# Kernel tuning notes

Hardware: AMD Instinct MI355X
Metric: run time of the kernel (lower is better)

Reference implementation:

```python
import jax, jax.numpy as jnp
import numpy as np

N0, N1, N2, C = 100_000, 400_000, 300_000, 128
NNZ1, NNZ2 = 2 * N1, 3 * N2  # 2 boundary nodes per edge, 3 boundary edges per triangle


def setup_inputs() -> dict:
    key = jax.random.key(0)
    ks = jax.random.split(key, 11)
    x0 = jax.random.normal(ks[0], (N0, C), dtype=jnp.float32)
    x1 = jax.random.normal(ks[1], (N1, C), dtype=jnp.float32)
    x2 = jax.random.normal(ks[2], (N2, C), dtype=jnp.float32)  # unused by the math (rank-2 conv reads rank-1 feats)
    W1 = jax.random.normal(ks[3], (C, C), dtype=jnp.float32) / np.sqrt(C)
    W2 = jax.random.normal(ks[4], (C, C), dtype=jnp.float32) / np.sqrt(C)
    # COO of incidence B_1: (N0, N1); B_2: (N1, N2)
    b1_rows = jax.random.randint(ks[5], (NNZ1,), 0, N0, dtype=jnp.int32)
    b1_cols = jax.random.randint(ks[6], (NNZ1,), 0, N1, dtype=jnp.int32)
    b1_vals = jax.random.uniform(ks[7], (NNZ1,), dtype=jnp.float32)
    b2_rows = jax.random.randint(ks[8], (NNZ2,), 0, N1, dtype=jnp.int32)
    b2_cols = jax.random.randint(ks[9], (NNZ2,), 0, N2, dtype=jnp.int32)
    b2_vals = jax.random.uniform(ks[10], (NNZ2,), dtype=jnp.float32)
    return {"x0": x0, "x1": x1, "x2": x2, "W1": W1, "W2": W2,
            "b1_rows": b1_rows, "b1_cols": b1_cols, "b1_vals": b1_vals,
            "b2_rows": b2_rows, "b2_cols": b2_cols, "b2_vals": b2_vals}


def _conv_low_to_high(x, W, rows, cols, vals, n_out):
    # B_r^T @ (x @ W): rows index (r-1)-cells (source), cols index r-cells (dest).
    h = x @ W                              # (n_{r-1}, C) dense GEMM
    msg = h[rows] * vals[:, None]          # (nnz, C) gather + scale
    return jax.ops.segment_sum(msg, cols, num_segments=n_out)  # (n_r, C)


def reference(x0, x1, x2, W1, W2, b1_rows, b1_cols, b1_vals, b2_rows, b2_cols, b2_vals):
    # Aggregation of a single-message list with aggr_func="sum" is identity,
    # followed by the sigmoid update. Rank 0 has an empty message list (the
    # original torch code would crash there), so outputs are ranks 1..max_rank.
    out1 = jax.nn.sigmoid(_conv_low_to_high(x0, W1, b1_rows, b1_cols, b1_vals, N1))
    out2 = jax.nn.sigmoid(_conv_low_to_high(x1, W2, b2_rows, b2_cols, b2_vals, N2))
    return (out1, out2)
```

## Files before the change

### kernel.cpp

```cpp
#include <hip/hip_runtime.h>
#include <hip/hip_bf16.h>

#define CDIM 128
#define SCAN_CHUNK 2048

typedef __attribute__((ext_vector_type(4))) float f32x4;
typedef __attribute__((ext_vector_type(8))) short bf16x8;
typedef __attribute__((ext_vector_type(4))) short bf16x4;

__device__ __forceinline__ short f2bf(float f) {
    unsigned u = __float_as_uint(f);
    u += 0x7FFFu + ((u >> 16) & 1u);
    return (short)(u >> 16);
}


__global__ __launch_bounds__(256) void zero_ints(int* __restrict__ p, int n) {
    int i = blockIdx.x * 256 + threadIdx.x;
    for (; i < n; i += gridDim.x * 256) p[i] = 0;
}

__global__ __launch_bounds__(256) void hist_both(
    const int* __restrict__ c1, int nnz1, const int* __restrict__ c2, int nnz2,
    int n1, int* __restrict__ counts)
{
    const int gtid = blockIdx.x * 256 + threadIdx.x;
    const int gstride = gridDim.x * 256;
    for (int e = gtid; e < nnz1; e += gstride) atomicAdd(&counts[c1[e]], 1);
    for (int e = gtid; e < nnz2; e += gstride) atomicAdd(&counts[n1 + c2[e]], 1);
}

__global__ __launch_bounds__(256) void scan_chunks(const int* __restrict__ in, int* __restrict__ out,
                                                   int* __restrict__ bsums, int n) {
    __shared__ int wtot[4];
    const int t = threadIdx.x;
    const int base = blockIdx.x * SCAN_CHUNK + t * 8;
    int v[8]; int s = 0;
#pragma unroll
    for (int j = 0; j < 8; ++j) {
        int c = (base + j < n) ? in[base + j] : 0;
        v[j] = s; s += c;
    }
    const int lane = t & 63, w = t >> 6;
    int inc = s;
#pragma unroll
    for (int d = 1; d < 64; d <<= 1) {
        int o = __shfl_up(inc, d);
        if (lane >= d) inc += o;
    }
    if (lane == 63) wtot[w] = inc;
    __syncthreads();
    int off = inc - s;
    for (int i = 0; i < w; ++i) off += wtot[i];
#pragma unroll
    for (int j = 0; j < 8; ++j)
        if (base + j < n) out[base + j] = v[j] + off;
    if (t == 255) bsums[blockIdx.x] = off + s;
}

__global__ __launch_bounds__(256) void scan_finalize(int* __restrict__ row_ptr,
                                                     const int* __restrict__ bsums,
                                                     int* __restrict__ cursor, int n, int nnzT) {
    __shared__ int wsum[4];
    const int t = threadIdx.x, lane = t & 63, w = t >> 6;
    int s = 0;
    for (int i = t; i < (int)blockIdx.x; i += 256) s += bsums[i];
#pragma unroll
    for (int d = 1; d < 64; d <<= 1) s += __shfl_xor(s, d);
    if (lane == 0) wsum[w] = s;
    __syncthreads();
    const int off = wsum[0] + wsum[1] + wsum[2] + wsum[3];
    const int base = blockIdx.x * SCAN_CHUNK + t * 8;
#pragma unroll
    for (int j = 0; j < 8; ++j) {
        const int i = base + j;
        if (i < n) {
            int val = row_ptr[i] + off;
            row_ptr[i] = val;
            cursor[i] = val;
        }
    }
    if (blockIdx.x == 0 && t == 0) row_ptr[n] = nnzT;
}

__global__ __launch_bounds__(256) void scatter_gemm(
    const int* __restrict__ r1, const int* __restrict__ c1, const float* __restrict__ v1, int nnz1,
    const int* __restrict__ r2, const int* __restrict__ c2, const float* __restrict__ v2, int nnz2,
    int n1, int* __restrict__ cursor, unsigned long long* __restrict__ csr, int nscat,
    const float* __restrict__ x0, const float* __restrict__ W1, short* __restrict__ h0, int t0,
    const float* __restrict__ x1, const float* __restrict__ W2, short* __restrict__ h1, int t1,
    int g0)
{
    __shared__ short Bfrag[4][8][64][8];

    if ((int)blockIdx.x < nscat) {
        const int gtid = blockIdx.x * 256 + threadIdx.x;
        const int gstride = nscat * 256;
        for (int e = gtid; e < nnz1; e += gstride) {
            int p = atomicAdd(&cursor[c1[e]], 1);
            csr[p] = ((unsigned long long)__float_as_uint(__builtin_nontemporal_load(&v1[e])) << 32)
                     | (unsigned)__builtin_nontemporal_load(&r1[e]);
        }
        for (int e = gtid; e < nnz2; e += gstride) {
            int p = atomicAdd(&cursor[n1 + c2[e]], 1);
            csr[p] = ((unsigned long long)__float_as_uint(__builtin_nontemporal_load(&v2[e])) << 32)
                     | (unsigned)__builtin_nontemporal_load(&r2[e]);
        }
        return;
    }

    const int gb = blockIdx.x - nscat;
    const float* __restrict__ x; const float* __restrict__ W; short* __restrict__ h;
    int ntiles, bidx, nblk;
    const int ngemm = gridDim.x - nscat;
    if (gb < g0) { x = x0; W = W1; h = h0; ntiles = t0; bidx = gb;      nblk = g0; }
    else         { x = x1; W = W2; h = h1; ntiles = t1; bidx = gb - g0; nblk = ngemm - g0; }

    for (int slot = threadIdx.x; slot < 2048; slot += 256) {
        const int lane = slot & 63, nb = (slot >> 6) & 7, kk = slot >> 9;
        const int n  = nb * 16 + (lane & 15);
        const int k0 = kk * 32 + (lane >> 4) * 8;
        union { bf16x8 v; short s[8]; } f;
#pragma unroll
        for (int j = 0; j < 8; ++j) f.s[j] = f2bf(W[(k0 + j) * CDIM + n]);
        *(bf16x8*)&Bfrag[kk][nb][lane][0] = f.v;
    }
    __syncthreads();

    const int lane = threadIdx.x & 63;
    const int wid  = threadIdx.x >> 6;
    const int l15  = lane & 15;
    const int l4   = lane >> 4;

    for (int tile = bidx * 4 + wid; tile < ntiles; tile += nblk * 4) {
        const int rbase = tile << 4;
        const int row = rbase + l15;
        const float* __restrict__ xr = x + (long)row * CDIM + (l4 << 3);

        union { bf16x8 v; short s[8]; } X[4];
#pragma unroll
        for (int kk = 0; kk < 4; ++kk) {
            f32x4 a0 = __builtin_nontemporal_load((const f32x4*)(xr + kk * 32));
            f32x4 a1 = __builtin_nontemporal_load((const f32x4*)(xr + kk * 32 + 4));
#pragma unroll
            for (int j = 0; j < 4; ++j) { X[kk].s[j] = f2bf(a0[j]); X[kk].s[4 + j] = f2bf(a1[j]); }
        }

        f32x4 c[8];
#pragma unroll
        for (int nb = 0; nb < 8; ++nb) c[nb] = (f32x4){0.f, 0.f, 0.f, 0.f};
#pragma unroll
        for (int kk = 0; kk < 4; ++kk)
#pragma unroll
            for (int nb = 0; nb < 8; ++nb)
                c[nb] = __builtin_amdgcn_mfma_f32_16x16x32_bf16(
                            *(const bf16x8*)&Bfrag[kk][nb][lane][0], X[kk].v, c[nb], 0, 0, 0);

        short* __restrict__ hr = h + (long)row * CDIM + (l4 << 2);
#pragma unroll
        for (int nb = 0; nb < 8; ++nb) {
            bf16x4 p;
#pragma unroll
            for (int ri = 0; ri < 4; ++ri) p[ri] = f2bf(c[nb][ri]);
            *(bf16x4*)(hr + (nb << 4)) = p;
        }
    }
}

__global__ __launch_bounds__(256) void agg_all(
    const short* __restrict__ h0, const short* __restrict__ h1,
    const int* __restrict__ row_ptr, const unsigned long long* __restrict__ csr,
    float* __restrict__ out, int n1, int nnzT)
{
    const int lane = threadIdx.x & 63;
    const int wid  = threadIdx.x >> 6;
    const int g    = lane >> 4;
    const int t16  = lane & 15;
    const int r = blockIdx.x * 16 + wid * 4 + g;
    const short* __restrict__ h = (r < n1) ? h0 : h1;
    const int beg = row_ptr[r];
    const int end = row_ptr[r + 1];
    const int deg = end - beg;

    int fi = beg + t16; if (fi > nnzT - 1) fi = nnzT - 1;
    const unsigned long long my = __builtin_nontemporal_load(&csr[fi]);

    const int m = deg < 16 ? deg : 16;
    const int gbase = g << 4;
    float acc[8] = {0.f, 0.f, 0.f, 0.f, 0.f, 0.f, 0.f, 0.f};

    bf16x8 hv[8]; float vv[8];
#pragma unroll
    for (int j = 0; j < 8; ++j) {
        if (j < m) {
            unsigned long long pv = __shfl(my, gbase + j);
            vv[j] = __uint_as_float((unsigned)(pv >> 32));
            hv[j] = *(const bf16x8*)(h + (long)(unsigned)(pv & 0xffffffffu) * CDIM + (t16 << 3));
        }
    }
#pragma unroll
    for (int j = 0; j < 8; ++j) {
        if (j < m) {
            union { bf16x8 v; unsigned u[4]; } H; H.v = hv[j];
#pragma unroll
            for (int d = 0; d < 4; ++d) {
                acc[2 * d]     += vv[j] * __uint_as_float(H.u[d] << 16);
                acc[2 * d + 1] += vv[j] * __uint_as_float(H.u[d] & 0xffff0000u);
            }
        }
    }
    if (__any(m > 8)) {
#pragma unroll
        for (int j = 8; j < 16; ++j) {
            if (j < m) {
                unsigned long long pv = __shfl(my, gbase + j);
                vv[j - 8] = __uint_as_float((unsigned)(pv >> 32));
                hv[j - 8] = *(const bf16x8*)(h + (long)(unsigned)(pv & 0xffffffffu) * CDIM + (t16 << 3));
            }
        }
#pragma unroll
        for (int j = 8; j < 16; ++j) {
            if (j < m) {
                union { bf16x8 v; unsigned u[4]; } H; H.v = hv[j - 8];
#pragma unroll
                for (int d = 0; d < 4; ++d) {
                    acc[2 * d]     += vv[j - 8] * __uint_as_float(H.u[d] << 16);
                    acc[2 * d + 1] += vv[j - 8] * __uint_as_float(H.u[d] & 0xffff0000u);
                }
            }
        }
    }
    for (int i = beg + 16; i < end; ++i) {
        const unsigned long long pv = csr[i];
        const float val = __uint_as_float((unsigned)(pv >> 32));
        union { bf16x8 v; unsigned u[4]; } H;
        H.v = *(const bf16x8*)(h + (long)(unsigned)(pv & 0xffffffffu) * CDIM + (t16 << 3));
#pragma unroll
        for (int d = 0; d < 4; ++d) {
            acc[2 * d]     += val * __uint_as_float(H.u[d] << 16);
            acc[2 * d + 1] += val * __uint_as_float(H.u[d] & 0xffff0000u);
        }
    }

    f32x4 o0, o1;
#pragma unroll
    for (int j = 0; j < 4; ++j) {
        o0[j] = 1.0f / (1.0f + __expf(-acc[j]));
        o1[j] = 1.0f / (1.0f + __expf(-acc[4 + j]));
    }
    float* __restrict__ orow = out + (long)r * CDIM + (t16 << 3);
    __builtin_nontemporal_store(o0, (f32x4*)orow);
    __builtin_nontemporal_store(o1, (f32x4*)(orow + 4));
}


extern "C" void kernel_launch(void* const* d_in, const int* in_sizes, int n_in,
                              void* d_out, int out_size, void* d_ws, size_t ws_size,
                              hipStream_t stream) {
    const float* x0 = (const float*)d_in[0];
    const float* x1 = (const float*)d_in[1];
    const float* W1 = (const float*)d_in[3];
    const float* W2 = (const float*)d_in[4];
    const int*   b1r = (const int*)d_in[5];
    const int*   b1c = (const int*)d_in[6];
    const float* b1v = (const float*)d_in[7];
    const int*   b2r = (const int*)d_in[8];
    const int*   b2c = (const int*)d_in[9];
    const float* b2v = (const float*)d_in[10];
    const int nnz1 = in_sizes[5];
    const int nnz2 = in_sizes[8];
    const int n0 = in_sizes[0] / CDIM;
    const int n1 = in_sizes[1] / CDIM;
    const int n2 = in_sizes[2] / CDIM;
    const int N  = n1 + n2;
    const int nnzT = nnz1 + nnz2;

    int* counts  = (int*)d_ws;
    int* row_ptr = counts + N;
    int* cursor  = row_ptr + N + 1;
    int* bsums   = cursor + N;
    size_t iofs = (size_t)3 * N + 1 + 512;
    iofs = (iofs + 1) & ~(size_t)1;
    unsigned long long* csr = (unsigned long long*)((int*)d_ws + iofs);
    short* h0 = (short*)(csr + nnzT);
    short* h1 = h0 + (size_t)n0 * CDIM;

    float* out = (float*)d_out;

    const int nchunks = (N + SCAN_CHUNK - 1) / SCAN_CHUNK;

    zero_ints<<<1024, 256, 0, stream>>>(counts, N);
    hist_both<<<2048, 256, 0, stream>>>(b1c, nnz1, b2c, nnz2, n1, counts);
    scan_chunks<<<nchunks, 256, 0, stream>>>(counts, row_ptr, bsums, N);
    scan_finalize<<<nchunks, 256, 0, stream>>>(row_ptr, bsums, cursor, N, nnzT);

    const int t0 = n0 >> 4, t1 = n1 >> 4;
    const int nscat = 512;
    scatter_gemm<<<nscat + 2048, 256, 0, stream>>>(
        b1r, b1c, b1v, nnz1, b2r, b2c, b2v, nnz2, n1, cursor, csr, nscat,
        x0, W1, h0, t0, x1, W2, h1, t1, 416);

    agg_all<<<N >> 4, 256, 0, stream>>>(h0, h1, row_ptr, csr, out, n1, nnzT);
}
```

Baseline: 478.4 us.

## Record per-edge rank during histogram to replace scatter atomics

The histogram pass now stores each edge's atomicAdd return value as its rank within the destination segment. The scatter then computes positions as row_ptr plus rank without any atomics and runs as its own kernel. Before, it was fused alongside the GEMM blocks. This removes the second round of contended atomics and the cursor array, at the cost of writing and re-reading an nnz-sized rank array and losing overlap between scatter and GEMM.

```diff
diff --git a/kernel.cpp b/kernel.cpp
--- a/kernel.cpp
+++ b/kernel.cpp
@@ -20,14 +20,16 @@
     for (; i < n; i += gridDim.x * 256) p[i] = 0;
 }
 
-__global__ __launch_bounds__(256) void hist_both(
+__global__ __launch_bounds__(256) void hist_rank(
     const int* __restrict__ c1, int nnz1, const int* __restrict__ c2, int nnz2,
-    int n1, int* __restrict__ counts)
+    int n1, int* __restrict__ counts, int* __restrict__ rank)
 {
     const int gtid = blockIdx.x * 256 + threadIdx.x;
     const int gstride = gridDim.x * 256;
-    for (int e = gtid; e < nnz1; e += gstride) atomicAdd(&counts[c1[e]], 1);
-    for (int e = gtid; e < nnz2; e += gstride) atomicAdd(&counts[n1 + c2[e]], 1);
+    for (int e = gtid; e < nnz1; e += gstride)
+        rank[e] = atomicAdd(&counts[c1[e]], 1);
+    for (int e = gtid; e < nnz2; e += gstride)
+        rank[nnz1 + e] = atomicAdd(&counts[n1 + c2[e]], 1);
 }
 
 __global__ __launch_bounds__(256) void scan_chunks(const int* __restrict__ in, int* __restrict__ out,
@@ -60,7 +62,7 @@
 
 __global__ __launch_bounds__(256) void scan_finalize(int* __restrict__ row_ptr,
                                                      const int* __restrict__ bsums,
-                                                     int* __restrict__ cursor, int n, int nnzT) {
+                                                     int n, int nnzT) {
     __shared__ int wsum[4];
     const int t = threadIdx.x, lane = t & 63, w = t >> 6;
     int s = 0;
@@ -74,48 +76,42 @@
 #pragma unroll
     for (int j = 0; j < 8; ++j) {
         const int i = base + j;
-        if (i < n) {
-            int val = row_ptr[i] + off;
-            row_ptr[i] = val;
-            cursor[i] = val;
-        }
+        if (i < n) row_ptr[i] += off;
     }
     if (blockIdx.x == 0 && t == 0) row_ptr[n] = nnzT;
 }
 
-__global__ __launch_bounds__(256) void scatter_gemm(
+__global__ __launch_bounds__(256) void scatter_both(
     const int* __restrict__ r1, const int* __restrict__ c1, const float* __restrict__ v1, int nnz1,
     const int* __restrict__ r2, const int* __restrict__ c2, const float* __restrict__ v2, int nnz2,
-    int n1, int* __restrict__ cursor, unsigned long long* __restrict__ csr, int nscat,
+    int n1, const int* __restrict__ row_ptr, const int* __restrict__ rank,
+    unsigned long long* __restrict__ csr)
+{
+    const int gtid = blockIdx.x * 256 + threadIdx.x;
+    const int gstride = gridDim.x * 256;
+    for (int e = gtid; e < nnz1; e += gstride) {
+        int p = row_ptr[c1[e]] + rank[e];
+        csr[p] = ((unsigned long long)__float_as_uint(__builtin_nontemporal_load(&v1[e])) << 32)
+                 | (unsigned)__builtin_nontemporal_load(&r1[e]);
+    }
+    for (int e = gtid; e < nnz2; e += gstride) {
+        int p = row_ptr[n1 + c2[e]] + rank[nnz1 + e];
+        csr[p] = ((unsigned long long)__float_as_uint(__builtin_nontemporal_load(&v2[e])) << 32)
+                 | (unsigned)__builtin_nontemporal_load(&r2[e]);
+    }
+}
+
+__global__ __launch_bounds__(256) void gemm_all(
     const float* __restrict__ x0, const float* __restrict__ W1, short* __restrict__ h0, int t0,
     const float* __restrict__ x1, const float* __restrict__ W2, short* __restrict__ h1, int t1,
     int g0)
 {
-    __shared__ short Bfrag[4][8][64][8];
-
-    if ((int)blockIdx.x < nscat) {
-        const int gtid = blockIdx.x * 256 + threadIdx.x;
-        const int gstride = nscat * 256;
-        for (int e = gtid; e < nnz1; e += gstride) {
-            int p = atomicAdd(&cursor[c1[e]], 1);
-            csr[p] = ((unsigned long long)__float_as_uint(__builtin_nontemporal_load(&v1[e])) << 32)
-                     | (unsigned)__builtin_nontemporal_load(&r1[e]);
-        }
-        for (int e = gtid; e < nnz2; e += gstride) {
-            int p = atomicAdd(&cursor[n1 + c2[e]], 1);
-            csr[p] = ((unsigned long long)__float_as_uint(__builtin_nontemporal_load(&v2[e])) << 32)
-                     | (unsigned)__builtin_nontemporal_load(&r2[e]);
-        }
-        return;
-    }
-
-    const int gb = blockIdx.x - nscat;
     const float* __restrict__ x; const float* __restrict__ W; short* __restrict__ h;
     int ntiles, bidx, nblk;
-    const int ngemm = gridDim.x - nscat;
-    if (gb < g0) { x = x0; W = W1; h = h0; ntiles = t0; bidx = gb;      nblk = g0; }
-    else         { x = x1; W = W2; h = h1; ntiles = t1; bidx = gb - g0; nblk = ngemm - g0; }
-
+    if ((int)blockIdx.x < g0) { x = x0; W = W1; h = h0; ntiles = t0; bidx = blockIdx.x;       nblk = g0; }
+    else                      { x = x1; W = W2; h = h1; ntiles = t1; bidx = blockIdx.x - g0; nblk = gridDim.x - g0; }
+
+    __shared__ short Bfrag[4][8][64][8];
     for (int slot = threadIdx.x; slot < 2048; slot += 256) {
         const int lane = slot & 63, nb = (slot >> 6) & 7, kk = slot >> 9;
         const int n  = nb * 16 + (lane & 15);
@@ -277,9 +273,9 @@
 
     int* counts  = (int*)d_ws;
     int* row_ptr = counts + N;
-    int* cursor  = row_ptr + N + 1;
-    int* bsums   = cursor + N;
-    size_t iofs = (size_t)3 * N + 1 + 512;
+    int* rank    = row_ptr + N + 1;
+    int* bsums   = rank + nnzT;
+    size_t iofs = (size_t)2 * N + 1 + nnzT + 512;
     iofs = (iofs + 1) & ~(size_t)1;
     unsigned long long* csr = (unsigned long long*)((int*)d_ws + iofs);
     short* h0 = (short*)(csr + nnzT);
@@ -290,15 +286,14 @@
     const int nchunks = (N + SCAN_CHUNK - 1) / SCAN_CHUNK;
 
     zero_ints<<<1024, 256, 0, stream>>>(counts, N);
-    hist_both<<<2048, 256, 0, stream>>>(b1c, nnz1, b2c, nnz2, n1, counts);
+    hist_rank<<<2048, 256, 0, stream>>>(b1c, nnz1, b2c, nnz2, n1, counts, rank);
     scan_chunks<<<nchunks, 256, 0, stream>>>(counts, row_ptr, bsums, N);
-    scan_finalize<<<nchunks, 256, 0, stream>>>(row_ptr, bsums, cursor, N, nnzT);
+    scan_finalize<<<nchunks, 256, 0, stream>>>(row_ptr, bsums, N, nnzT);
+    scatter_both<<<2048, 256, 0, stream>>>(b1r, b1c, b1v, nnz1, b2r, b2c, b2v, nnz2,
+                                           n1, row_ptr, rank, csr);
 
     const int t0 = n0 >> 4, t1 = n1 >> 4;
-    const int nscat = 512;
-    scatter_gemm<<<nscat + 2048, 256, 0, stream>>>(
-        b1r, b1c, b1v, nnz1, b2r, b2c, b2v, nnz2, n1, cursor, csr, nscat,
-        x0, W1, h0, t0, x1, W2, h1, t1, 416);
+    gemm_all<<<2048, 256, 0, stream>>>(x0, W1, h0, t0, x1, W2, h1, t1, 416);
 
     agg_all<<<N >> 4, 256, 0, stream>>>(h0, h1, row_ptr, csr, out, n1, nnzT);
 }
```

Result: faster. 400.4 us, median of 2 (-16.3%).
